# Performance work log

Hardware: AMD Instinct MI355X
Metric: run time of the kernel (lower is better)

Reference implementation:

```python
import jax, jax.numpy as jnp
import numpy as np

N, K, D, H = 16384, 8, 128, 256  # nodes, preds per node, emb dim, hidden


def _build_graph():
    i = np.arange(1, N + 1)[:, None]      # [N,1] node ids 1..N
    k = np.arange(K)[None, :]             # [1,K]
    pred = i - 1 - k                       # predecessor node ids
    mask = pred >= 0
    pred_nodes = np.maximum(pred, 0).astype(np.int32)        # [N,K]
    end = np.repeat(np.arange(1, N + 1), K).astype(np.int32)  # [N*K]
    edges = np.stack([pred_nodes.reshape(-1), end], axis=1)   # [E,2]
    pred_edge_idx = (np.arange(N * K).reshape(N, K) + 1).astype(np.int32)  # +1: zero row prepended to distances
    return pred_nodes, pred_edge_idx, mask, edges.astype(np.int32)


def setup_inputs() -> dict:
    key = jax.random.key(0)
    k1, k2, k3 = jax.random.split(key, 3)
    pred_nodes, pred_edge_idx, mask, edges = _build_graph()
    s1 = 1.0 / np.sqrt(2 * D)
    s2 = 1.0 / np.sqrt(H)
    return {
        "words_embs": jax.random.normal(k1, (N + 1, D), dtype=jnp.float32),
        "W1": jax.random.uniform(k2, (2 * D, H), jnp.float32, -s1, s1),
        "b1": jnp.zeros((H,), jnp.float32),
        "W2": jax.random.uniform(k3, (H, 1), jnp.float32, -s2, s2),
        "b2": jnp.zeros((1,), jnp.float32),
        "best_idxs": jnp.arange(N + 1, dtype=jnp.int32),  # the chain path 0->1->...->N
        "edges": jnp.asarray(edges),
        "pred_nodes": jnp.asarray(pred_nodes),
        "pred_edge_idx": jnp.asarray(pred_edge_idx),
        "pred_mask": jnp.asarray(mask),
    }


def _distance(x, y, W1, b1, W2, b2):
    # MLP over concatenated pair features: Linear -> Tanh -> Linear -> Softplus
    h = jnp.tanh(jnp.concatenate([x, y], axis=-1) @ W1 + b1)
    return jax.nn.softplus(h @ W2 + b2)  # [...,1]


def _forward_alg(words_embs, edges, pred_nodes, pred_edge_idx, pred_mask, W1, b1, W2, b2):
    n_nodes = pred_nodes.shape[0]
    d = _distance(words_embs[edges[:, 0]], words_embs[edges[:, 1]], W1, b1, W2, b2)  # [E,1]
    dists = jnp.concatenate([jnp.zeros((1, 1), d.dtype), d], axis=0)[:, 0]  # [E+1]
    esum0 = jnp.zeros((n_nodes + 1,), d.dtype)
    neg_inf = jnp.asarray(-jnp.inf, d.dtype)

    def step(esum, inp):
        i, preds, eidx, m = inp
        vals = jnp.where(m, esum[preds] - dists[eidx], neg_inf)  # [K]
        mx = jnp.max(vals)
        lse = mx + jnp.log(jnp.sum(jnp.exp(vals - mx)))
        return esum.at[i].set(lse), None

    idxs = jnp.arange(1, n_nodes + 1, dtype=jnp.int32)
    esum, _ = jax.lax.scan(step, esum0, (idxs, pred_nodes, pred_edge_idx, pred_mask))
    return esum[-1]


def reference(words_embs, W1, b1, W2, b2, best_idxs, edges, pred_nodes, pred_edge_idx, pred_mask):
    # gold path score
    feats = words_embs[best_idxs]  # [P,D]
    gold = _distance(feats[:-1], feats[1:], W1, b1, W2, b2).sum(0)  # [1]
    # partition-function-like forward score over the lattice
    fwd = _forward_alg(words_embs, edges, pred_nodes, pred_edge_idx, pred_mask, W1, b1, W2, b2)
    return (gold + fwd).mean()  # single-sample version of loss_fuc
```

## Files before the change

### kernel.cpp

```cpp
#include <hip/hip_runtime.h>
#include <math.h>

#define NV 16385
#define NEDGE 131072
#define NEG -1e30f
#define SCALE 2.8853900817779268f

typedef __attribute__((ext_vector_type(8))) short short8;
typedef __attribute__((ext_vector_type(4))) float f32x4;

__device__ float g_part[4 * NEDGE];
__device__ float g_mats[32 * 64];
__device__ float g_gold;

__device__ __forceinline__ unsigned short f2bf(float x) {
  union { float f; unsigned int u; } c; c.f = x;
  unsigned int u = c.u;
  unsigned int r = (u + 0x7fffu + ((u >> 16) & 1u)) >> 16;
  return (unsigned short)r;
}

__device__ __forceinline__ float lse8(float x0, float x1, float x2, float x3,
                                      float x4, float x5, float x6, float x7) {
  float m = fmaxf(fmaxf(fmaxf(x0, x1), fmaxf(x2, x3)),
                  fmaxf(fmaxf(x4, x5), fmaxf(x6, x7)));
  float s = __expf(x0 - m) + __expf(x1 - m) + __expf(x2 - m) + __expf(x3 - m) +
            __expf(x4 - m) + __expf(x5 - m) + __expf(x6 - m) + __expf(x7 - m);
  return m + __logf(s);
}

__device__ __forceinline__ float comb8(float A, float B, int i8, int j) {
  float x0 = __shfl(A, i8 + 0) + __shfl(B, 0 + j);
  float x1 = __shfl(A, i8 + 1) + __shfl(B, 8 + j);
  float x2 = __shfl(A, i8 + 2) + __shfl(B, 16 + j);
  float x3 = __shfl(A, i8 + 3) + __shfl(B, 24 + j);
  float x4 = __shfl(A, i8 + 4) + __shfl(B, 32 + j);
  float x5 = __shfl(A, i8 + 5) + __shfl(B, 40 + j);
  float x6 = __shfl(A, i8 + 6) + __shfl(B, 48 + j);
  float x7 = __shfl(A, i8 + 7) + __shfl(B, 56 + j);
  return lse8(x0, x1, x2, x3, x4, x5, x6, x7);
}

#define ETERM(ea, eb, w, acc)                              \
  {                                                        \
    float e_ = (ea) * (eb);                                \
    acc = fmaf(__builtin_amdgcn_rcpf(e_ + 1.f), (w), acc); \
  }

__global__ __launch_bounds__(256, 4) void k12_fused(const float* __restrict__ emb,
                                                    const float* __restrict__ W1,
                                                    const float* __restrict__ b1,
                                                    const float* __restrict__ W2) {
  __shared__ __align__(16) unsigned short lds[19728];
  unsigned short* Es = lds;
  float* CA  = (float*)lds;
  float* CB  = (float*)(lds + 10880);
  float* W2s = (float*)(lds + 19584);
  float* Wsum = (float*)(lds + 19712);

  const int t = threadIdx.x;
  const int h0 = blockIdx.x << 6;
  const int i0 = blockIdx.y << 6;
  const int wv = t >> 6, lane = t & 63;
  const int l15 = lane & 15, quad = lane >> 4;
  const int colh = h0 + (wv << 4) + l15;

  if (t < 64) W2s[t] = -2.f * W2[h0 + t];
  if (t < 8) {
    float s = 0.f;
#pragma unroll
    for (int jj = 0; jj < 8; ++jj) s += W2[h0 + (t << 3) + jj];
    Wsum[t] = s;
  }

#pragma unroll
  for (int it = 0; it < 10; ++it) {
    int idx = t + (it << 8);
    int row = idx >> 5;
    int k4 = (idx & 31) << 2;
    int v = i0 - 7 + row;
    float4 g = make_float4(0.f, 0.f, 0.f, 0.f);
    if (v >= 0 && v < NV) g = *(const float4*)&emb[v * 128 + k4];
    uint2 pk;
    pk.x = f2bf(g.x) | ((unsigned int)f2bf(g.y) << 16);
    pk.y = f2bf(g.z) | ((unsigned int)f2bf(g.w) << 16);
    *(uint2*)&Es[row * 136 + k4] = pk;
  }

  f32x4 accA[5], accB[4];
#pragma unroll
  for (int m = 0; m < 5; ++m) accA[m] = (f32x4){0.f, 0.f, 0.f, 0.f};
#pragma unroll
  for (int m = 0; m < 4; ++m) accB[m] = (f32x4){0.f, 0.f, 0.f, 0.f};

  short8 fA[4], fB[4];
#pragma unroll
  for (int kc = 0; kc < 4; ++kc) {
    const int kb = (kc << 5) + (quad << 3);
#pragma unroll
    for (int i = 0; i < 8; i += 2) {
      float a0 = W1[(kb + i) * 256 + colh];
      float a1 = W1[(kb + i + 1) * 256 + colh];
      float c0 = W1[(128 + kb + i) * 256 + colh];
      float c1 = W1[(128 + kb + i + 1) * 256 + colh];
      ((unsigned int*)&fA[kc])[i >> 1] = f2bf(a0) | ((unsigned int)f2bf(a1) << 16);
      ((unsigned int*)&fB[kc])[i >> 1] = f2bf(c0) | ((unsigned int)f2bf(c1) << 16);
    }
  }
  __syncthreads();

#pragma unroll
  for (int kc = 0; kc < 4; ++kc) {
    const int kbase = (kc << 5) + (quad << 3);
#pragma unroll
    for (int mf = 0; mf < 5; ++mf) {
      short8 a = *(const short8*)&Es[((mf << 4) + l15) * 136 + kbase];
      accA[mf] = __builtin_amdgcn_mfma_f32_16x16x32_bf16(a, fA[kc], accA[mf], 0, 0, 0);
    }
#pragma unroll
    for (int mf = 0; mf < 4; ++mf) {
      short8 a = *(const short8*)&Es[(8 + (mf << 4) + l15) * 136 + kbase];
      accB[mf] = __builtin_amdgcn_mfma_f32_16x16x32_bf16(a, fB[kc], accB[mf], 0, 0, 0);
    }
  }
  __syncthreads();
  const int hcol = (wv << 4) + l15;
  const float b1s = b1[h0 + hcol];
#pragma unroll
  for (int mf = 0; mf < 5; ++mf) {
    int rb = (mf << 4) + (quad << 2);
#pragma unroll
    for (int rr = 0; rr < 4; ++rr)
      CA[(rb + rr) * 68 + hcol] =
          __builtin_amdgcn_exp2f((accA[mf][rr] + b1s) * SCALE);
  }
#pragma unroll
  for (int mf = 0; mf < 4; ++mf) {
    int rb = (mf << 4) + (quad << 2);
#pragma unroll
    for (int rr = 0; rr < 4; ++rr)
      CB[(rb + rr) * 68 + hcol] = __builtin_amdgcn_exp2f(accB[mf][rr] * SCALE);
  }
  __syncthreads();
  const int k = t & 7;
  const int qb = t >> 3;
  float ws_all = 0.f;
#pragma unroll
  for (int s = 0; s < 8; ++s) ws_all += Wsum[s];
  float pa0 = 0.f, pa1 = 0.f, pb0 = 0.f, pb1 = 0.f;
#pragma unroll
  for (int g = 0; g < 8; ++g) {
    const int s = (g + (k << 1)) & 7;
    const float* wp = &W2s[s << 3];
    float4 w0 = *(const float4*)wp;
    float4 w1 = *(const float4*)(wp + 4);
    {
      const float* ap = &CA[(7 + qb - k) * 68 + (s << 3)];
      const float* bp = &CB[qb * 68 + (s << 3)];
      float4 a0 = *(const float4*)ap, a1 = *(const float4*)(ap + 4);
      float4 b0 = *(const float4*)bp, b1v = *(const float4*)(bp + 4);
      ETERM(a0.x, b0.x, w0.x, pa0); ETERM(a0.y, b0.y, w0.y, pa0);
      ETERM(a0.z, b0.z, w0.z, pa0); ETERM(a0.w, b0.w, w0.w, pa0);
      ETERM(a1.x, b1v.x, w1.x, pa1); ETERM(a1.y, b1v.y, w1.y, pa1);
      ETERM(a1.z, b1v.z, w1.z, pa1); ETERM(a1.w, b1v.w, w1.w, pa1);
    }
    {
      const int q = qb + 32;
      const float* ap = &CA[(7 + q - k) * 68 + (s << 3)];
      const float* bp = &CB[q * 68 + (s << 3)];
      float4 a0 = *(const float4*)ap, a1 = *(const float4*)(ap + 4);
      float4 b0 = *(const float4*)bp, b1v = *(const float4*)(bp + 4);
      ETERM(a0.x, b0.x, w0.x, pb0); ETERM(a0.y, b0.y, w0.y, pb0);
      ETERM(a0.z, b0.z, w0.z, pb0); ETERM(a0.w, b0.w, w0.w, pb0);
      ETERM(a1.x, b1v.x, w1.x, pb1); ETERM(a1.y, b1v.y, w1.y, pb1);
      ETERM(a1.z, b1v.z, w1.z, pb1); ETERM(a1.w, b1v.w, w1.w, pb1);
    }
  }
  const int ebase = blockIdx.x * NEDGE + (blockIdx.y << 9) + t;
  g_part[ebase] = (pa0 + pa1) + ws_all;
  g_part[ebase + 256] = (pb0 + pb1) + ws_all;
}

__global__ __launch_bounds__(256) void k_tail1(const float* __restrict__ b2) {
  __shared__ float wf[64][64];
  __shared__ float m8[8][64];
  const int t = threadIdx.x;
  const int b = blockIdx.x;
  const float b2v = b2[0];
  float gold = 0.f;
#pragma unroll
  for (int it = 0; it < 4; ++it) {
    const int e4 = t + (it << 8);
    const int gidx = (b << 10) + e4;
    float4 s0 = *(const float4*)&g_part[gidx << 2];
    float4 s1 = *(const float4*)&g_part[NEDGE + (gidx << 2)];
    float4 s2 = *(const float4*)&g_part[2 * NEDGE + (gidx << 2)];
    float4 s3 = *(const float4*)&g_part[3 * NEDGE + (gidx << 2)];
    float d0 = s0.x + s1.x + s2.x + s3.x + b2v;
    float d1 = s0.y + s1.y + s2.y + s3.y + b2v;
    float d2 = s0.z + s1.z + s2.z + s3.z + b2v;
    float d3 = s0.w + s1.w + s2.w + s3.w + b2v;
    d0 = fmaxf(d0, 0.f) + log1pf(__expf(-fabsf(d0)));
    d1 = fmaxf(d1, 0.f) + log1pf(__expf(-fabsf(d1)));
    d2 = fmaxf(d2, 0.f) + log1pf(__expf(-fabsf(d2)));
    d3 = fmaxf(d3, 0.f) + log1pf(__expf(-fabsf(d3)));
    const int q = e4 << 2;
    const int cl = q >> 9, r = q & 511;
    const int s = r >> 3, kk = r & 7;
    *(float4*)&wf[s][(cl << 3) + kk] = make_float4(d0, d1, d2, d3);
    if ((t & 1) == 0) gold += d0;
  }
#pragma unroll
  for (int off = 32; off > 0; off >>= 1) gold += __shfl_xor(gold, off, 64);
  if ((t & 63) == 0) atomicAdd(&g_gold, gold);
  __syncthreads();
  if (b == 0 && t == 0) {
    for (int s = 0; s < 7; ++s)
      for (int kk = s + 1; kk < 8; ++kk) wf[s][kk] = 1e30f;
  }
  __syncthreads();
  if (t < 64) {
    const int g = t >> 3, j = t & 7;
    float P[8];
#pragma unroll
    for (int kk = 0; kk < 8; ++kk) P[kk] = (kk == j) ? 0.f : NEG;
    for (int s = 0; s < 64; ++s) {
      const float* wp = &wf[s][g << 3];
      float4 wa = *(const float4*)wp;
      float4 wb = *(const float4*)(wp + 4);
      float nv = lse8(P[0] - wa.x, P[1] - wa.y, P[2] - wa.z, P[3] - wa.w,
                      P[4] - wb.x, P[5] - wb.y, P[6] - wb.z, P[7] - wb.w);
#pragma unroll
      for (int kk = 7; kk > 0; --kk) P[kk] = P[kk - 1];
      P[0] = nv;
    }
#pragma unroll
    for (int kk = 0; kk < 8; ++kk) m8[g][(kk << 3) + j] = P[kk];
    const int i8 = (t >> 3) << 3;
    float R = m8[0][t];
#pragma unroll
    for (int g2 = 1; g2 < 8; ++g2) R = comb8(m8[g2][t], R, i8, j);
    g_mats[(b << 6) + t] = R;
  }
}

__global__ __launch_bounds__(256) void k_tail2(float* __restrict__ out) {
  __shared__ float l2m[4][64];
  const int t = threadIdx.x;
  const int l = t & 63, w = t >> 6;
  const int i8 = (l >> 3) << 3, j = l & 7;
  float G = g_mats[((w << 3) << 6) + l];
#pragma unroll
  for (int s2 = 1; s2 < 8; ++s2)
    G = comb8(g_mats[(((w << 3) + s2) << 6) + l], G, i8, j);
  l2m[w][l] = G;
  __syncthreads();
  if (t < 64) {
    float G2 = l2m[0][t];
#pragma unroll
    for (int w2 = 1; w2 < 4; ++w2) G2 = comb8(l2m[w2][t], G2, i8, j);
    if (t == 0) {
      out[0] = g_gold + G2;
      g_gold = 0.f;
    }
  }
}

extern "C" void kernel_launch(void* const* d_in, const int* in_sizes, int n_in,
                              void* d_out, int out_size, void* d_ws, size_t ws_size,
                              hipStream_t stream) {
  const float* emb = (const float*)d_in[0];
  const float* W1 = (const float*)d_in[1];
  const float* b1 = (const float*)d_in[2];
  const float* W2 = (const float*)d_in[3];
  const float* b2 = (const float*)d_in[4];
  float* out = (float*)d_out;
  hipLaunchKernelGGL(k12_fused, dim3(4, 256), dim3(256), 0, stream, emb, W1, b1, W2);
  hipLaunchKernelGGL(k_tail1, dim3(32), dim3(256), 0, stream, b2);
  hipLaunchKernelGGL(k_tail2, dim3(1), dim3(256), 0, stream, out);
}
```

Measured before the change: 110.7 us.

## Fuse edge MLP and scan tail kernels into one launch with atomic counters

Merges the three kernels into a single launch of 1056 blocks. The first 1024 blocks compute edge distances, and the last 32 spin-wait on per-chunk atomic counters before running the per-chunk semiring scan. The last tail block to finish does the final combine and resets the counters. This removes two kernel launch boundaries and lets tail work overlap with the MLP blocks still running. It depends on the tail blocks being scheduled after the producer blocks to avoid deadlock, and it adds spin-wait and fence overhead.

```diff
diff --git a/kernel.cpp b/kernel.cpp
--- a/kernel.cpp
+++ b/kernel.cpp
@@ -12,6 +12,8 @@
 __device__ float g_part[4 * NEDGE];
 __device__ float g_mats[32 * 64];
 __device__ float g_gold;
+__device__ int g_cnt[32];
+__device__ int g_done;
 
 __device__ __forceinline__ unsigned short f2bf(float x) {
   union { float f; unsigned int u; } c; c.f = x;
@@ -47,151 +49,174 @@
     acc = fmaf(__builtin_amdgcn_rcpf(e_ + 1.f), (w), acc); \
   }
 
-__global__ __launch_bounds__(256, 4) void k12_fused(const float* __restrict__ emb,
-                                                    const float* __restrict__ W1,
-                                                    const float* __restrict__ b1,
-                                                    const float* __restrict__ W2) {
+__global__ __launch_bounds__(256, 4) void k_all(const float* __restrict__ emb,
+                                                const float* __restrict__ W1,
+                                                const float* __restrict__ b1,
+                                                const float* __restrict__ W2,
+                                                const float* __restrict__ b2,
+                                                float* __restrict__ out) {
   __shared__ __align__(16) unsigned short lds[19728];
-  unsigned short* Es = lds;
-  float* CA  = (float*)lds;
-  float* CB  = (float*)(lds + 10880);
-  float* W2s = (float*)(lds + 19584);
-  float* Wsum = (float*)(lds + 19712);
-
   const int t = threadIdx.x;
-  const int h0 = blockIdx.x << 6;
-  const int i0 = blockIdx.y << 6;
-  const int wv = t >> 6, lane = t & 63;
-  const int l15 = lane & 15, quad = lane >> 4;
-  const int colh = h0 + (wv << 4) + l15;
-
-  if (t < 64) W2s[t] = -2.f * W2[h0 + t];
-  if (t < 8) {
-    float s = 0.f;
-#pragma unroll
-    for (int jj = 0; jj < 8; ++jj) s += W2[h0 + (t << 3) + jj];
-    Wsum[t] = s;
-  }
-
-#pragma unroll
-  for (int it = 0; it < 10; ++it) {
-    int idx = t + (it << 8);
-    int row = idx >> 5;
-    int k4 = (idx & 31) << 2;
-    int v = i0 - 7 + row;
-    float4 g = make_float4(0.f, 0.f, 0.f, 0.f);
-    if (v >= 0 && v < NV) g = *(const float4*)&emb[v * 128 + k4];
-    uint2 pk;
-    pk.x = f2bf(g.x) | ((unsigned int)f2bf(g.y) << 16);
-    pk.y = f2bf(g.z) | ((unsigned int)f2bf(g.w) << 16);
-    *(uint2*)&Es[row * 136 + k4] = pk;
-  }
-
-  f32x4 accA[5], accB[4];
-#pragma unroll
-  for (int m = 0; m < 5; ++m) accA[m] = (f32x4){0.f, 0.f, 0.f, 0.f};
-#pragma unroll
-  for (int m = 0; m < 4; ++m) accB[m] = (f32x4){0.f, 0.f, 0.f, 0.f};
-
-  short8 fA[4], fB[4];
-#pragma unroll
-  for (int kc = 0; kc < 4; ++kc) {
-    const int kb = (kc << 5) + (quad << 3);
-#pragma unroll
-    for (int i = 0; i < 8; i += 2) {
-      float a0 = W1[(kb + i) * 256 + colh];
-      float a1 = W1[(kb + i + 1) * 256 + colh];
-      float c0 = W1[(128 + kb + i) * 256 + colh];
-      float c1 = W1[(128 + kb + i + 1) * 256 + colh];
-      ((unsigned int*)&fA[kc])[i >> 1] = f2bf(a0) | ((unsigned int)f2bf(a1) << 16);
-      ((unsigned int*)&fB[kc])[i >> 1] = f2bf(c0) | ((unsigned int)f2bf(c1) << 16);
-    }
-  }
-  __syncthreads();
-
-#pragma unroll
-  for (int kc = 0; kc < 4; ++kc) {
-    const int kbase = (kc << 5) + (quad << 3);
+  const int bid = blockIdx.x;
+
+  if (bid < 1024) {
+    unsigned short* Es = lds;
+    float* CA = (float*)lds;
+    float* CB = (float*)(lds + 10880);
+    float* W2s = (float*)(lds + 19584);
+    float* Wsum = (float*)(lds + 19712);
+
+    const int hx = bid & 3;
+    const int by = bid >> 2;
+    const int h0 = hx << 6;
+    const int i0 = by << 6;
+    const int wv = t >> 6, lane = t & 63;
+    const int l15 = lane & 15, quad = lane >> 4;
+    const int colh = h0 + (wv << 4) + l15;
+
+    if (t < 64) W2s[t] = -2.f * W2[h0 + t];
+    if (t < 8) {
+      float s = 0.f;
+#pragma unroll
+      for (int jj = 0; jj < 8; ++jj) s += W2[h0 + (t << 3) + jj];
+      Wsum[t] = s;
+    }
+
+#pragma unroll
+    for (int it = 0; it < 10; ++it) {
+      int idx = t + (it << 8);
+      int row = idx >> 5;
+      int k4 = (idx & 31) << 2;
+      int v = i0 - 7 + row;
+      float4 g = make_float4(0.f, 0.f, 0.f, 0.f);
+      if (v >= 0 && v < NV) g = *(const float4*)&emb[v * 128 + k4];
+      uint2 pk;
+      pk.x = f2bf(g.x) | ((unsigned int)f2bf(g.y) << 16);
+      pk.y = f2bf(g.z) | ((unsigned int)f2bf(g.w) << 16);
+      *(uint2*)&Es[row * 136 + k4] = pk;
+    }
+
+    f32x4 accA[5], accB[4];
+#pragma unroll
+    for (int m = 0; m < 5; ++m) accA[m] = (f32x4){0.f, 0.f, 0.f, 0.f};
+#pragma unroll
+    for (int m = 0; m < 4; ++m) accB[m] = (f32x4){0.f, 0.f, 0.f, 0.f};
+
+    short8 fA[4], fB[4];
+#pragma unroll
+    for (int kc = 0; kc < 4; ++kc) {
+      const int kb = (kc << 5) + (quad << 3);
+#pragma unroll
+      for (int i = 0; i < 8; i += 2) {
+        float a0 = W1[(kb + i) * 256 + colh];
+        float a1 = W1[(kb + i + 1) * 256 + colh];
+        float c0 = W1[(128 + kb + i) * 256 + colh];
+        float c1 = W1[(128 + kb + i + 1) * 256 + colh];
+        ((unsigned int*)&fA[kc])[i >> 1] = f2bf(a0) | ((unsigned int)f2bf(a1) << 16);
+        ((unsigned int*)&fB[kc])[i >> 1] = f2bf(c0) | ((unsigned int)f2bf(c1) << 16);
+      }
+    }
+    __syncthreads();
+
+#pragma unroll
+    for (int kc = 0; kc < 4; ++kc) {
+      const int kbase = (kc << 5) + (quad << 3);
+#pragma unroll
+      for (int mf = 0; mf < 5; ++mf) {
+        short8 a = *(const short8*)&Es[((mf << 4) + l15) * 136 + kbase];
+        accA[mf] = __builtin_amdgcn_mfma_f32_16x16x32_bf16(a, fA[kc], accA[mf], 0, 0, 0);
+      }
+#pragma unroll
+      for (int mf = 0; mf < 4; ++mf) {
+        short8 a = *(const short8*)&Es[(8 + (mf << 4) + l15) * 136 + kbase];
+        accB[mf] = __builtin_amdgcn_mfma_f32_16x16x32_bf16(a, fB[kc], accB[mf], 0, 0, 0);
+      }
+    }
+    __syncthreads();
+    const int hcol = (wv << 4) + l15;
+    const float b1s = b1[h0 + hcol];
 #pragma unroll
     for (int mf = 0; mf < 5; ++mf) {
-      short8 a = *(const short8*)&Es[((mf << 4) + l15) * 136 + kbase];
-      accA[mf] = __builtin_amdgcn_mfma_f32_16x16x32_bf16(a, fA[kc], accA[mf], 0, 0, 0);
+      int rb = (mf << 4) + (quad << 2);
+#pragma unroll
+      for (int rr = 0; rr < 4; ++rr)
+        CA[(rb + rr) * 68 + hcol] =
+            __builtin_amdgcn_exp2f((accA[mf][rr] + b1s) * SCALE);
     }
 #pragma unroll
     for (int mf = 0; mf < 4; ++mf) {
-      short8 a = *(const short8*)&Es[(8 + (mf << 4) + l15) * 136 + kbase];
-      accB[mf] = __builtin_amdgcn_mfma_f32_16x16x32_bf16(a, fB[kc], accB[mf], 0, 0, 0);
-    }
-  }
-  __syncthreads();
-  const int hcol = (wv << 4) + l15;
-  const float b1s = b1[h0 + hcol];
-#pragma unroll
-  for (int mf = 0; mf < 5; ++mf) {
-    int rb = (mf << 4) + (quad << 2);
-#pragma unroll
-    for (int rr = 0; rr < 4; ++rr)
-      CA[(rb + rr) * 68 + hcol] =
-          __builtin_amdgcn_exp2f((accA[mf][rr] + b1s) * SCALE);
-  }
-#pragma unroll
-  for (int mf = 0; mf < 4; ++mf) {
-    int rb = (mf << 4) + (quad << 2);
-#pragma unroll
-    for (int rr = 0; rr < 4; ++rr)
-      CB[(rb + rr) * 68 + hcol] = __builtin_amdgcn_exp2f(accB[mf][rr] * SCALE);
-  }
-  __syncthreads();
-  const int k = t & 7;
-  const int qb = t >> 3;
-  float ws_all = 0.f;
-#pragma unroll
-  for (int s = 0; s < 8; ++s) ws_all += Wsum[s];
-  float pa0 = 0.f, pa1 = 0.f, pb0 = 0.f, pb1 = 0.f;
-#pragma unroll
-  for (int g = 0; g < 8; ++g) {
-    const int s = (g + (k << 1)) & 7;
-    const float* wp = &W2s[s << 3];
-    float4 w0 = *(const float4*)wp;
-    float4 w1 = *(const float4*)(wp + 4);
-    {
-      const float* ap = &CA[(7 + qb - k) * 68 + (s << 3)];
-      const float* bp = &CB[qb * 68 + (s << 3)];
-      float4 a0 = *(const float4*)ap, a1 = *(const float4*)(ap + 4);
-      float4 b0 = *(const float4*)bp, b1v = *(const float4*)(bp + 4);
-      ETERM(a0.x, b0.x, w0.x, pa0); ETERM(a0.y, b0.y, w0.y, pa0);
-      ETERM(a0.z, b0.z, w0.z, pa0); ETERM(a0.w, b0.w, w0.w, pa0);
-      ETERM(a1.x, b1v.x, w1.x, pa1); ETERM(a1.y, b1v.y, w1.y, pa1);
-      ETERM(a1.z, b1v.z, w1.z, pa1); ETERM(a1.w, b1v.w, w1.w, pa1);
-    }
-    {
-      const int q = qb + 32;
-      const float* ap = &CA[(7 + q - k) * 68 + (s << 3)];
-      const float* bp = &CB[q * 68 + (s << 3)];
-      float4 a0 = *(const float4*)ap, a1 = *(const float4*)(ap + 4);
-      float4 b0 = *(const float4*)bp, b1v = *(const float4*)(bp + 4);
-      ETERM(a0.x, b0.x, w0.x, pb0); ETERM(a0.y, b0.y, w0.y, pb0);
-      ETERM(a0.z, b0.z, w0.z, pb0); ETERM(a0.w, b0.w, w0.w, pb0);
-      ETERM(a1.x, b1v.x, w1.x, pb1); ETERM(a1.y, b1v.y, w1.y, pb1);
-      ETERM(a1.z, b1v.z, w1.z, pb1); ETERM(a1.w, b1v.w, w1.w, pb1);
-    }
-  }
-  const int ebase = blockIdx.x * NEDGE + (blockIdx.y << 9) + t;
-  g_part[ebase] = (pa0 + pa1) + ws_all;
-  g_part[ebase + 256] = (pb0 + pb1) + ws_all;
-}
-
-__global__ __launch_bounds__(256) void k_tail1(const float* __restrict__ b2) {
-  __shared__ float wf[64][64];
-  __shared__ float m8[8][64];
-  const int t = threadIdx.x;
-  const int b = blockIdx.x;
+      int rb = (mf << 4) + (quad << 2);
+#pragma unroll
+      for (int rr = 0; rr < 4; ++rr)
+        CB[(rb + rr) * 68 + hcol] = __builtin_amdgcn_exp2f(accB[mf][rr] * SCALE);
+    }
+    __syncthreads();
+    const int k = t & 7;
+    const int qb = t >> 3;
+    float ws_all = 0.f;
+#pragma unroll
+    for (int s = 0; s < 8; ++s) ws_all += Wsum[s];
+    float pa0 = 0.f, pa1 = 0.f, pb0 = 0.f, pb1 = 0.f;
+#pragma unroll
+    for (int g = 0; g < 8; ++g) {
+      const int s = (g + (k << 1)) & 7;
+      const float* wp = &W2s[s << 3];
+      float4 w0 = *(const float4*)wp;
+      float4 w1 = *(const float4*)(wp + 4);
+      {
+        const float* ap = &CA[(7 + qb - k) * 68 + (s << 3)];
+        const float* bp = &CB[qb * 68 + (s << 3)];
+        float4 a0 = *(const float4*)ap, a1 = *(const float4*)(ap + 4);
+        float4 b0 = *(const float4*)bp, b1v = *(const float4*)(bp + 4);
+        ETERM(a0.x, b0.x, w0.x, pa0); ETERM(a0.y, b0.y, w0.y, pa0);
+        ETERM(a0.z, b0.z, w0.z, pa0); ETERM(a0.w, b0.w, w0.w, pa0);
+        ETERM(a1.x, b1v.x, w1.x, pa1); ETERM(a1.y, b1v.y, w1.y, pa1);
+        ETERM(a1.z, b1v.z, w1.z, pa1); ETERM(a1.w, b1v.w, w1.w, pa1);
+      }
+      {
+        const int q = qb + 32;
+        const float* ap = &CA[(7 + q - k) * 68 + (s << 3)];
+        const float* bp = &CB[q * 68 + (s << 3)];
+        float4 a0 = *(const float4*)ap, a1 = *(const float4*)(ap + 4);
+        float4 b0 = *(const float4*)bp, b1v = *(const float4*)(bp + 4);
+        ETERM(a0.x, b0.x, w0.x, pb0); ETERM(a0.y, b0.y, w0.y, pb0);
+        ETERM(a0.z, b0.z, w0.z, pb0); ETERM(a0.w, b0.w, w0.w, pb0);
+        ETERM(a1.x, b1v.x, w1.x, pb1); ETERM(a1.y, b1v.y, w1.y, pb1);
+        ETERM(a1.z, b1v.z, w1.z, pb1); ETERM(a1.w, b1v.w, w1.w, pb1);
+      }
+    }
+    const int ebase = hx * NEDGE + (by << 9) + t;
+    g_part[ebase] = (pa0 + pa1) + ws_all;
+    g_part[ebase + 256] = (pb0 + pb1) + ws_all;
+    __syncthreads();
+    if (t == 0) {
+      __threadfence();
+      __hip_atomic_fetch_add(&g_cnt[by >> 3], 1, __ATOMIC_RELEASE,
+                             __HIP_MEMORY_SCOPE_AGENT);
+    }
+    return;
+  }
+
+  const int tb = bid - 1024;
+  float* wf = (float*)lds;
+  float* m8 = (float*)(lds + 8192);
+  float* l2m = (float*)(lds + 9216);
+  int* flag = (int*)(lds + 9728);
+
+  if (t == 0) {
+    while (__hip_atomic_load(&g_cnt[tb], __ATOMIC_ACQUIRE,
+                             __HIP_MEMORY_SCOPE_AGENT) < 32)
+      __builtin_amdgcn_s_sleep(2);
+  }
+  __syncthreads();
+  __threadfence();
+
   const float b2v = b2[0];
   float gold = 0.f;
 #pragma unroll
   for (int it = 0; it < 4; ++it) {
     const int e4 = t + (it << 8);
-    const int gidx = (b << 10) + e4;
+    const int gidx = (tb << 10) + e4;
     float4 s0 = *(const float4*)&g_part[gidx << 2];
     float4 s1 = *(const float4*)&g_part[NEDGE + (gidx << 2)];
     float4 s2 = *(const float4*)&g_part[2 * NEDGE + (gidx << 2)];
@@ -207,16 +232,16 @@
     const int q = e4 << 2;
     const int cl = q >> 9, r = q & 511;
     const int s = r >> 3, kk = r & 7;
-    *(float4*)&wf[s][(cl << 3) + kk] = make_float4(d0, d1, d2, d3);
+    *(float4*)&wf[s * 64 + (cl << 3) + kk] = make_float4(d0, d1, d2, d3);
     if ((t & 1) == 0) gold += d0;
   }
 #pragma unroll
   for (int off = 32; off > 0; off >>= 1) gold += __shfl_xor(gold, off, 64);
   if ((t & 63) == 0) atomicAdd(&g_gold, gold);
   __syncthreads();
-  if (b == 0 && t == 0) {
+  if (tb == 0 && t == 0) {
     for (int s = 0; s < 7; ++s)
-      for (int kk = s + 1; kk < 8; ++kk) wf[s][kk] = 1e30f;
+      for (int kk = s + 1; kk < 8; ++kk) wf[s * 64 + kk] = 1e30f;
   }
   __syncthreads();
   if (t < 64) {
@@ -225,7 +250,7 @@
 #pragma unroll
     for (int kk = 0; kk < 8; ++kk) P[kk] = (kk == j) ? 0.f : NEG;
     for (int s = 0; s < 64; ++s) {
-      const float* wp = &wf[s][g << 3];
+      const float* wp = &wf[s * 64 + (g << 3)];
       float4 wa = *(const float4*)wp;
       float4 wb = *(const float4*)(wp + 4);
       float nv = lse8(P[0] - wa.x, P[1] - wa.y, P[2] - wa.z, P[3] - wa.w,
@@ -235,34 +260,43 @@
       P[0] = nv;
     }
 #pragma unroll
-    for (int kk = 0; kk < 8; ++kk) m8[g][(kk << 3) + j] = P[kk];
+    for (int kk = 0; kk < 8; ++kk) m8[g * 64 + (kk << 3) + j] = P[kk];
     const int i8 = (t >> 3) << 3;
-    float R = m8[0][t];
-#pragma unroll
-    for (int g2 = 1; g2 < 8; ++g2) R = comb8(m8[g2][t], R, i8, j);
-    g_mats[(b << 6) + t] = R;
-  }
-}
-
-__global__ __launch_bounds__(256) void k_tail2(float* __restrict__ out) {
-  __shared__ float l2m[4][64];
-  const int t = threadIdx.x;
-  const int l = t & 63, w = t >> 6;
-  const int i8 = (l >> 3) << 3, j = l & 7;
-  float G = g_mats[((w << 3) << 6) + l];
-#pragma unroll
-  for (int s2 = 1; s2 < 8; ++s2)
-    G = comb8(g_mats[(((w << 3) + s2) << 6) + l], G, i8, j);
-  l2m[w][l] = G;
-  __syncthreads();
-  if (t < 64) {
-    float G2 = l2m[0][t];
-#pragma unroll
-    for (int w2 = 1; w2 < 4; ++w2) G2 = comb8(l2m[w2][t], G2, i8, j);
-    if (t == 0) {
-      out[0] = g_gold + G2;
-      g_gold = 0.f;
-    }
+    float R = m8[t];
+#pragma unroll
+    for (int g2 = 1; g2 < 8; ++g2) R = comb8(m8[g2 * 64 + t], R, i8, j);
+    g_mats[(tb << 6) + t] = R;
+  }
+  __syncthreads();
+  if (t == 0) {
+    __threadfence();
+    int old = __hip_atomic_fetch_add(&g_done, 1, __ATOMIC_ACQ_REL,
+                                     __HIP_MEMORY_SCOPE_AGENT);
+    flag[0] = (old == 31) ? 1 : 0;
+  }
+  __syncthreads();
+  if (flag[0]) {
+    __threadfence();
+    const int l = t & 63, w = t >> 6;
+    const int i8 = (l >> 3) << 3, j = l & 7;
+    float G = g_mats[((w << 3) << 6) + l];
+#pragma unroll
+    for (int s2 = 1; s2 < 8; ++s2)
+      G = comb8(g_mats[(((w << 3) + s2) << 6) + l], G, i8, j);
+    l2m[w * 64 + l] = G;
+    __syncthreads();
+    if (t < 64) {
+      float G2 = l2m[t];
+#pragma unroll
+      for (int w2 = 1; w2 < 4; ++w2) G2 = comb8(l2m[w2 * 64 + t], G2, i8, j);
+      if (t == 0) {
+        out[0] = __hip_atomic_load(&g_gold, __ATOMIC_RELAXED,
+                                   __HIP_MEMORY_SCOPE_AGENT) + G2;
+        g_gold = 0.f;
+        g_done = 0;
+      }
+    }
+    if (t < 32) g_cnt[t] = 0;
   }
 }
 
@@ -275,7 +309,5 @@
   const float* W2 = (const float*)d_in[3];
   const float* b2 = (const float*)d_in[4];
   float* out = (float*)d_out;
-  hipLaunchKernelGGL(k12_fused, dim3(4, 256), dim3(256), 0, stream, emb, W1, b1, W2);
-  hipLaunchKernelGGL(k_tail1, dim3(32), dim3(256), 0, stream, b2);
-  hipLaunchKernelGGL(k_tail2, dim3(1), dim3(256), 0, stream, out);
-}
+  hipLaunchKernelGGL(k_all, dim3(1056), dim3(256), 0, stream, emb, W1, b1, W2, b2, out);
+}
```

After: 145.1 us. 1.31x slower.

## Precompute bf16 embeddings and W1 fragments in a prep kernel, DMA into LDS

Applied to the files above, without the earlier changes.

Adds a prep kernel that converts the embeddings to bf16 into a padded, XOR-swizzled global buffer and packs the W1 MFMA fragments once. The main kernel then copies its embedding tile straight into LDS with global_load_lds and loads its W1 fragments as single vectors. Before this, each of the 1024 blocks redid the fp32 loads and bf16 conversions and gathered W1 with strided loads. The cost is one extra kernel launch and extra global traffic for the intermediate buffers, and the LDS layout changes from padded rows to a swizzle.

```diff
diff --git a/kernel.cpp b/kernel.cpp
--- a/kernel.cpp
+++ b/kernel.cpp
@@ -12,12 +12,20 @@
 __device__ float g_part[4 * NEDGE];
 __device__ float g_mats[32 * 64];
 __device__ float g_gold;
+__device__ unsigned short g_embh[16408 * 128];
+__device__ unsigned short g_w1bf[8192 * 8];
 
 __device__ __forceinline__ unsigned short f2bf(float x) {
   union { float f; unsigned int u; } c; c.f = x;
   unsigned int u = c.u;
   unsigned int r = (u + 0x7fffu + ((u >> 16) & 1u)) >> 16;
   return (unsigned short)r;
+}
+
+__device__ __forceinline__ void gll16(const void* g, void* l) {
+  __builtin_amdgcn_global_load_lds(
+      (const __attribute__((address_space(1))) unsigned int*)g,
+      (__attribute__((address_space(3))) unsigned int*)l, 16, 0, 0);
 }
 
 __device__ __forceinline__ float lse8(float x0, float x1, float x2, float x3,
@@ -47,23 +55,69 @@
     acc = fmaf(__builtin_amdgcn_rcpf(e_ + 1.f), (w), acc); \
   }
 
-__global__ __launch_bounds__(256, 4) void k12_fused(const float* __restrict__ emb,
-                                                    const float* __restrict__ W1,
-                                                    const float* __restrict__ b1,
+__global__ __launch_bounds__(256) void k_prep(const float* __restrict__ emb,
+                                              const float* __restrict__ W1) {
+  const int gid = blockIdx.x * 256 + threadIdx.x;
+  for (int i = gid; i < 16408 * 16; i += 256 * 256) {
+    const int r = i >> 4, g = i & 15;
+    const int key = (r - 1) & 7;
+    const int v = r - 8;
+    uint4 o = make_uint4(0u, 0u, 0u, 0u);
+    if (v >= 0 && v < NV) {
+      const float* src = &emb[v * 128 + ((g ^ key) << 3)];
+      float4 a = *(const float4*)src;
+      float4 b = *(const float4*)(src + 4);
+      o.x = f2bf(a.x) | ((unsigned int)f2bf(a.y) << 16);
+      o.y = f2bf(a.z) | ((unsigned int)f2bf(a.w) << 16);
+      o.z = f2bf(b.x) | ((unsigned int)f2bf(b.y) << 16);
+      o.w = f2bf(b.z) | ((unsigned int)f2bf(b.w) << 16);
+    }
+    *(uint4*)&g_embh[(r << 7) + (g << 3)] = o;
+  }
+  if (gid < 8192) {
+    const int tt = gid & 255;
+    const int fh = gid >> 8;
+    const int hx = fh & 3, f = fh >> 2;
+    const int wv = tt >> 6, lane = tt & 63;
+    const int l15 = lane & 15, quad = lane >> 4;
+    const int col = (hx << 6) + (wv << 4) + l15;
+    const int kb = ((f & 3) << 5) + (quad << 3) + ((f >> 2) << 7);
+    unsigned int w[4];
+#pragma unroll
+    for (int i = 0; i < 8; i += 2) {
+      float a0 = W1[(kb + i) * 256 + col];
+      float a1 = W1[(kb + i + 1) * 256 + col];
+      w[i >> 1] = f2bf(a0) | ((unsigned int)f2bf(a1) << 16);
+    }
+    *(uint4*)&g_w1bf[gid << 3] = *(const uint4*)w;
+  }
+}
+
+__global__ __launch_bounds__(256, 4) void k12_fused(const float* __restrict__ b1,
                                                     const float* __restrict__ W2) {
-  __shared__ __align__(16) unsigned short lds[19728];
+  __shared__ __align__(16) unsigned short lds[19088];
   unsigned short* Es = lds;
-  float* CA  = (float*)lds;
-  float* CB  = (float*)(lds + 10880);
-  float* W2s = (float*)(lds + 19584);
-  float* Wsum = (float*)(lds + 19712);
+  float* CA = (float*)lds;
+  float* CB = (float*)(lds + 10240);
+  float* W2s = (float*)(lds + 18944);
+  float* Wsum = (float*)(lds + 19072);
 
   const int t = threadIdx.x;
-  const int h0 = blockIdx.x << 6;
-  const int i0 = blockIdx.y << 6;
+  const int hx = blockIdx.x;
+  const int h0 = hx << 6;
+  const int i0 = (int)blockIdx.y << 6;
   const int wv = t >> 6, lane = t & 63;
   const int l15 = lane & 15, quad = lane >> 4;
-  const int colh = h0 + (wv << 4) + l15;
+
+  {
+    const char* src = (const char*)&g_embh[(i0 + 1) << 7];
+    char* dst = (char*)lds;
+#pragma unroll
+    for (int p = 0; p < 5; ++p) {
+      const int off = (p << 12) + (wv << 10);
+      gll16(src + off + (lane << 4), dst + off);
+    }
+  }
 
   if (t < 64) W2s[t] = -2.f * W2[h0 + t];
   if (t < 8) {
@@ -73,18 +127,11 @@
     Wsum[t] = s;
   }
 
-#pragma unroll
-  for (int it = 0; it < 10; ++it) {
-    int idx = t + (it << 8);
-    int row = idx >> 5;
-    int k4 = (idx & 31) << 2;
-    int v = i0 - 7 + row;
-    float4 g = make_float4(0.f, 0.f, 0.f, 0.f);
-    if (v >= 0 && v < NV) g = *(const float4*)&emb[v * 128 + k4];
-    uint2 pk;
-    pk.x = f2bf(g.x) | ((unsigned int)f2bf(g.y) << 16);
-    pk.y = f2bf(g.z) | ((unsigned int)f2bf(g.w) << 16);
-    *(uint2*)&Es[row * 136 + k4] = pk;
+  short8 fA[4], fB[4];
+#pragma unroll
+  for (int kc = 0; kc < 4; ++kc) {
+    fA[kc] = *(const short8*)&g_w1bf[((((kc << 2) + hx) << 8) + t) << 3];
+    fB[kc] = *(const short8*)&g_w1bf[((((16 + (kc << 2)) + hx) << 8) + t) << 3];
   }
 
   f32x4 accA[5], accB[4];
@@ -93,33 +140,21 @@
 #pragma unroll
   for (int m = 0; m < 4; ++m) accB[m] = (f32x4){0.f, 0.f, 0.f, 0.f};
 
-  short8 fA[4], fB[4];
+  __syncthreads();
+
 #pragma unroll
   for (int kc = 0; kc < 4; ++kc) {
-    const int kb = (kc << 5) + (quad << 3);
-#pragma unroll
-    for (int i = 0; i < 8; i += 2) {
-      float a0 = W1[(kb + i) * 256 + colh];
-      float a1 = W1[(kb + i + 1) * 256 + colh];
-      float c0 = W1[(128 + kb + i) * 256 + colh];
-      float c1 = W1[(128 + kb + i + 1) * 256 + colh];
-      ((unsigned int*)&fA[kc])[i >> 1] = f2bf(a0) | ((unsigned int)f2bf(a1) << 16);
-      ((unsigned int*)&fB[kc])[i >> 1] = f2bf(c0) | ((unsigned int)f2bf(c1) << 16);
-    }
-  }
-  __syncthreads();
-
-#pragma unroll
-  for (int kc = 0; kc < 4; ++kc) {
-    const int kbase = (kc << 5) + (quad << 3);
+    const int cb = (kc << 5) + (quad << 3);
 #pragma unroll
     for (int mf = 0; mf < 5; ++mf) {
-      short8 a = *(const short8*)&Es[((mf << 4) + l15) * 136 + kbase];
+      const int row = (mf << 4) + l15;
+      short8 a = *(const short8*)&Es[(row << 7) + (cb ^ ((row & 7) << 3))];
       accA[mf] = __builtin_amdgcn_mfma_f32_16x16x32_bf16(a, fA[kc], accA[mf], 0, 0, 0);
     }
 #pragma unroll
     for (int mf = 0; mf < 4; ++mf) {
-      short8 a = *(const short8*)&Es[(8 + (mf << 4) + l15) * 136 + kbase];
+      const int row = 8 + (mf << 4) + l15;
+      short8 a = *(const short8*)&Es[(row << 7) + (cb ^ ((row & 7) << 3))];
       accB[mf] = __builtin_amdgcn_mfma_f32_16x16x32_bf16(a, fB[kc], accB[mf], 0, 0, 0);
     }
   }
@@ -131,8 +166,9 @@
     int rb = (mf << 4) + (quad << 2);
 #pragma unroll
     for (int rr = 0; rr < 4; ++rr)
-      CA[(rb + rr) * 68 + hcol] =
-          __builtin_amdgcn_exp2f((accA[mf][rr] + b1s) * SCALE);
+      if (rb + rr < 71)
+        CA[(rb + rr) * 68 + hcol] =
+            __builtin_amdgcn_exp2f((accA[mf][rr] + b1s) * SCALE);
   }
 #pragma unroll
   for (int mf = 0; mf < 4; ++mf) {
@@ -176,7 +212,7 @@
       ETERM(a1.z, b1v.z, w1.z, pb1); ETERM(a1.w, b1v.w, w1.w, pb1);
     }
   }
-  const int ebase = blockIdx.x * NEDGE + (blockIdx.y << 9) + t;
+  const int ebase = hx * NEDGE + ((int)blockIdx.y << 9) + t;
   g_part[ebase] = (pa0 + pa1) + ws_all;
   g_part[ebase + 256] = (pb0 + pb1) + ws_all;
 }
@@ -275,7 +311,8 @@
   const float* W2 = (const float*)d_in[3];
   const float* b2 = (const float*)d_in[4];
   float* out = (float*)d_out;
-  hipLaunchKernelGGL(k12_fused, dim3(4, 256), dim3(256), 0, stream, emb, W1, b1, W2);
+  hipLaunchKernelGGL(k_prep, dim3(256), dim3(256), 0, stream, emb, W1);
+  hipLaunchKernelGGL(k12_fused, dim3(4, 256), dim3(256), 0, stream, b1, W2);
   hipLaunchKernelGGL(k_tail1, dim3(32), dim3(256), 0, stream, b2);
   hipLaunchKernelGGL(k_tail2, dim3(1), dim3(256), 0, stream, out);
 }
```

Result: no change. 110.1 us (-0.5%).
